# Kernel optimization log

Hardware: AMD Instinct MI355X
Metric: run time of the kernel (lower is better)

Reference implementation:

```python
import jax, jax.numpy as jnp
import numpy as np

HIDDEN = 3072
HEADS = 32
HEAD_DIM = HIDDEN // HEADS  # 96


def setup_inputs() -> dict:
    key = jax.random.key(0)
    k1, k2, k3, k4 = jax.random.split(key, 4)
    B, S = 2, 2048
    x = jax.random.normal(k1, (B, S, HIDDEN), dtype=jnp.float32)
    # qkv_proj: Linear(hidden, 3*hidden, bias=False); torch weight is [out,in]
    w_qkv = jax.random.normal(k2, (3 * HIDDEN, HIDDEN), dtype=jnp.float32) * (HIDDEN ** -0.5)
    # o_proj: Linear(hidden, hidden) with bias
    w_o = jax.random.normal(k3, (HIDDEN, HIDDEN), dtype=jnp.float32) * (HIDDEN ** -0.5)
    b_o = jax.random.normal(k4, (HIDDEN,), dtype=jnp.float32) * 0.01
    return {"x": x, "w_qkv": w_qkv, "w_o": w_o, "b_o": b_o}


def reference(x, w_qkv, w_o, b_o):
    B, S, _ = x.shape
    qkv = jnp.einsum('bsh,oh->bso', x, w_qkv)  # [B,S,3*HIDDEN]
    q, k, v = jnp.split(qkv, 3, axis=-1)
    # [B,S,HIDDEN] -> [B,H,S,D]
    def split_heads(t):
        return t.reshape(B, S, HEADS, HEAD_DIM).transpose(0, 2, 1, 3)
    q, k, v = split_heads(q), split_heads(k), split_heads(v)
    scores = jnp.einsum('bhqd,bhkd->bhqk', q, k) / jnp.sqrt(jnp.float32(HEAD_DIM))
    attn = jax.nn.softmax(scores, axis=-1)
    out = jnp.einsum('bhqk,bhkd->bhqd', attn, v)  # [B,H,S,D]
    out = out.transpose(0, 2, 1, 3).reshape(B, S, HIDDEN)
    return jnp.einsum('bsh,oh->bso', out, w_o) + b_o
```

## Files before the change

kernel.cpp:

```cpp
#include <hip/hip_runtime.h>
#include <math.h>


typedef unsigned int u32;
typedef unsigned short u16;
typedef __attribute__((ext_vector_type(8))) short bf16x8;
typedef __attribute__((ext_vector_type(4))) float f32x4;
typedef __attribute__((ext_vector_type(16))) float f32x16;

#define MFMA(a, b, c) __builtin_amdgcn_mfma_f32_16x16x32_bf16((a), (b), (c), 0, 0, 0)
#define MFMA32(a, b, c) __builtin_amdgcn_mfma_f32_32x32x16_bf16((a), (b), (c), 0, 0, 0)

#define GLDS16(g, l) __builtin_amdgcn_global_load_lds( \
    (const __attribute__((address_space(1))) u32*)(g), \
    (__attribute__((address_space(3))) u32*)(l), 16, 0, 0)

__device__ __forceinline__ u16 f2bf(float f) {
  u32 u = __builtin_bit_cast(u32, f);
  return (u16)((u + 0x7fffu + ((u >> 16) & 1u)) >> 16);
}
__device__ __forceinline__ float bf2f(u16 h) {
  u32 u = ((u32)h) << 16;
  return __builtin_bit_cast(float, u);
}
__device__ __forceinline__ void split2(float f, u16& h, u16& l) {
  h = f2bf(f);
  l = f2bf(f - bf2f(h));
}
__device__ __forceinline__ bf16x8 ld16(const u16* p) {
  return *reinterpret_cast<const bf16x8*>(p);
}

__global__ void split_kernel(const float* __restrict__ src, u16* __restrict__ dst,
                             long n) {
  long i = ((long)blockIdx.x * 256 + threadIdx.x) * 4;
  if (i >= n) return;
  const float4 v = *reinterpret_cast<const float4*>(src + i);
  const u32 i32 = (u32)i;
  const u32 row = i32 / 3072u;
  const u32 col = i32 - row * 3072u;
  const long base = (long)row * 6144 + (col >> 5) * 64 + (col & 31);
  ushort4 h, l;
  split2(v.x, h.x, l.x);
  split2(v.y, h.y, l.y);
  split2(v.z, h.z, l.z);
  split2(v.w, h.w, l.w);
  *reinterpret_cast<ushort4*>(dst + base) = h;
  *reinterpret_cast<ushort4*>(dst + base + 32) = l;
}

template <int MODE>
__global__ __launch_bounds__(256, 2) void gemm32(
    const u16* __restrict__ A2, const u16* __restrict__ B2,
    int M, int N, u16* __restrict__ C2, u16* __restrict__ Kp,
    u16* __restrict__ Vp, float* __restrict__ Cf, const float* __restrict__ bias) {
  constexpr int NT = 96;
  __shared__ u16 shm[2 * 128 * 64 + 2 * 192 * 64];
  u16* const uA = shm;
  u16* const uB = shm + 2 * 128 * 64;
  const int tid = threadIdx.x;
  const int lane = tid & 63;
  const int w = tid >> 6;
  const int wm = w >> 1, wn = w & 1;
  const int l31 = lane & 31;
  const int l5 = lane >> 5;

  const int mt = M >> 7;
  const int nwg = gridDim.x;
  const int bid = blockIdx.x;
  const int wg = (bid & 7) * (nwg >> 3) + (bid >> 3);
  const int bm = wg % mt, bn = wg / mt;

  const int srow = lane >> 3;
  const int sgc = ((lane & 7) ^ srow ^ w) * 8;

  auto stA = [&](int buf, int kt, int j) {
    const int r = j * 32 + w * 8 + srow;
    GLDS16(A2 + (long)(bm * 128 + r) * 6144 + kt * 64 + sgc,
           &uA[buf * 8192 + (j * 32 + w * 8) * 64]);
  };
  auto stB = [&](int buf, int kt, int j) {
    const int r = j * 32 + w * 8 + srow;
    GLDS16(B2 + (long)(bn * 192 + r) * 6144 + kt * 64 + sgc,
           &uB[buf * 12288 + (j * 32 + w * 8) * 64]);
  };

  f32x16 acc[2][3];
#pragma unroll
  for (int m = 0; m < 2; ++m)
#pragma unroll
    for (int n = 0; n < 3; ++n)
#pragma unroll
      for (int j = 0; j < 16; ++j) acc[m][n][j] = 0.f;

  stA(0, 0, 0); stA(0, 0, 1); stA(0, 0, 2); stA(0, 0, 3);
  stB(0, 0, 0); stB(0, 0, 1); stB(0, 0, 2);
  stB(0, 0, 3); stB(0, 0, 4); stB(0, 0, 5);
  __syncthreads();

  const int aRow0 = wm * 64 + l31;
  const int bRow0 = wn * 96 + l31;
  const int rk = (lane & 7) ^ ((lane >> 3) & 3);

#define CSLOT(KS, PL) ((((KS)*2 + l5 + (PL)*4) ^ rk) * 8)
#define RD_PH(KS)                                                          \
  _Pragma("unroll") for (int n = 0; n < 3; ++n) {                          \
    const int off = (bRow0 + n * 32) * 64;                                 \
    b[n][0] = ld16(&LB[off + CSLOT(KS, 0)]);                               \
    b[n][1] = ld16(&LB[off + CSLOT(KS, 1)]);                               \
  }                                                                        \
  _Pragma("unroll") for (int m = 0; m < 2; ++m) {                          \
    const int off = (aRow0 + m * 32) * 64;                                 \
    a[m][0] = ld16(&LA[off + CSLOT(KS, 0)]);                               \
    a[m][1] = ld16(&LA[off + CSLOT(KS, 1)]);                               \
  }
#define DO_MFMA3()                                                         \
  __builtin_amdgcn_s_setprio(1);                                           \
  _Pragma("unroll") for (int m = 0; m < 2; ++m)                            \
  _Pragma("unroll") for (int n = 0; n < 3; ++n) {                          \
    acc[m][n] = MFMA32(a[m][0], b[n][0], acc[m][n]);                       \
    acc[m][n] = MFMA32(a[m][0], b[n][1], acc[m][n]);                       \
    acc[m][n] = MFMA32(a[m][1], b[n][0], acc[m][n]);                       \
  }                                                                        \
  __builtin_amdgcn_s_setprio(0);
#define PH_SYNC()                                                          \
  __builtin_amdgcn_s_barrier();                                            \
  asm volatile("s_waitcnt lgkmcnt(0)" ::: "memory");                       \
  __builtin_amdgcn_sched_barrier(0);

  for (int t = 0; t < NT; ++t) {
    const int cur = t & 1;
    const int nxt = cur ^ 1;
    const u16* LA = &uA[cur * 8192];
    const u16* LB = &uB[cur * 12288];
    bf16x8 a[2][2], b[3][2];
    RD_PH(0);
    if (t + 1 < NT) {
      stA(nxt, t + 1, 0); stA(nxt, t + 1, 1);
      stA(nxt, t + 1, 2); stA(nxt, t + 1, 3);
      stB(nxt, t + 1, 0); stB(nxt, t + 1, 1); stB(nxt, t + 1, 2);
      stB(nxt, t + 1, 3); stB(nxt, t + 1, 4); stB(nxt, t + 1, 5);
    }
    PH_SYNC();
    DO_MFMA3();
    __builtin_amdgcn_s_barrier();
    RD_PH(1);
    PH_SYNC();
    DO_MFMA3();
    asm volatile("s_waitcnt vmcnt(0)" ::: "memory");
    __builtin_amdgcn_s_barrier();
  }
#undef CSLOT
#undef RD_PH
#undef DO_MFMA3
#undef PH_SYNC

  if (MODE == 1 || (MODE == 2 && bn < 16)) {
#pragma unroll
    for (int mf = 0; mf < 2; ++mf)
#pragma unroll
      for (int nf = 0; nf < 3; ++nf) {
        const int col = bn * 192 + wn * 96 + nf * 32 + l31;
#pragma unroll
        for (int reg = 0; reg < 16; ++reg) {
          const int rif = (reg & 3) + 8 * (reg >> 2) + 4 * l5;
          const long row = (long)bm * 128 + wm * 64 + mf * 32 + rif;
          const float v = acc[mf][nf][reg];
          if (MODE == 1) {
            Cf[row * N + col] = v + bias[col];
          } else {
            const long idx = row * 6144 + (col >> 5) * 64 + (col & 31);
            u16 h, l;
            split2(v, h, l);
            C2[idx] = h;
            C2[idx + 32] = l;
          }
        }
      }
  } else if (MODE == 2) {
    const bool isV = (bn >= 32);
    const int hd0 = (bn - (isV ? 32 : 16)) * 2;
    const int b = (bm * 128) >> 11;
    const int s_loc = (bm * 128) & 2047;
    u16* const P = shm;
    u16* const dst = isV ? Vp : Kp;
#pragma unroll
    for (int hf = 0; hf < 2; ++hf) {
      __syncthreads();
      if (wm == hf) {
#pragma unroll
        for (int mf = 0; mf < 2; ++mf)
#pragma unroll
          for (int nf = 0; nf < 3; ++nf)
#pragma unroll
            for (int reg = 0; reg < 16; ++reg) {
              const int rif = (reg & 3) + 8 * (reg >> 2) + 4 * l5;
              const int row_l = mf * 32 + rif;
              const int col_l = wn * 96 + nf * 32 + l31;
              u16 h, l;
              split2(acc[mf][nf][reg], h, l);
              P[row_l * 200 + col_l] = h;
              P[(64 + row_l) * 200 + col_l] = l;
            }
      }
      __syncthreads();
      const int lr = lane & 15, lg = lane >> 4;
      if (!isV) {
#pragma unroll
        for (int i = 0; i < 12; ++i) {
          const int ri = w * 12 + i;
          const int pl = ri & 1;
          const int kbi = (ri >> 1) & 3;
          const int c = (ri >> 3) % 3;
          const int hh = ri / 24;
          const bf16x8 v =
              ld16(&P[(pl * 64 + kbi * 16 + lr) * 200 + hh * 96 + c * 32 + lg * 8]);
          const int hl = b * 32 + hd0 + hh;
          const int kbg = ((s_loc + hf * 64) >> 4) + kbi;
          const long rec3 = ((long)hl * 128 + kbg) * 3 + c;
          *reinterpret_cast<bf16x8*>(dst + (rec3 * 2 + pl) * 512 + lane * 8) = v;
        }
      } else {
#pragma unroll
        for (int i = 0; i < 12; ++i) {
          const int ri = w * 12 + i;
          const int pl = ri & 1;
          const int kq = (ri >> 1) & 1;
          const int n = (ri >> 2) % 6;
          const int hh = ri / 24;
          bf16x8 v;
#pragma unroll
          for (int e = 0; e < 8; ++e)
            v[e] = (short)P[(pl * 64 + kq * 32 + lg * 8 + e) * 200 + hh * 96 + n * 16 + lr];
          const int hl = b * 32 + hd0 + hh;
          const int kqg = ((s_loc + hf * 64) >> 5) + kq;
          const long rec = (((long)hl * 6 + n) * 64 + kqg) * 2 + pl;
          *reinterpret_cast<bf16x8*>(dst + rec * 512 + lane * 8) = v;
        }
      }
    }
  }
}

__global__ __launch_bounds__(256, 2) void attn_kernel(
    const u16* __restrict__ Q2,
    const u16* __restrict__ Kp, const u16* __restrict__ Vp,
    u16* __restrict__ AO2) {
  __shared__ u16 kv[2][12 * 512];
  __shared__ u16 pb[4][2][2][512];
  const int lane = threadIdx.x & 63;
  const int wv = threadIdx.x >> 6;
  const int lr = lane & 15, lg = lane >> 4;

  const int nwg = gridDim.x;
  const int bid = blockIdx.x;
  const int wg = (bid & 7) * (nwg >> 3) + (bid >> 3);
  const int hl = wg >> 4;
  const int qblk = wg & 15;
  const int b = hl >> 5;
  const int q0 = qblk * 128 + wv * 32;

  bf16x8 qh[2][3], ql[2][3];
#pragma unroll
  for (int f = 0; f < 2; ++f) {
    const long qofs =
        ((long)(b * 2048 + q0 + f * 16 + lr)) * 6144 + ((hl & 31) * 3) * 64 + lg * 8;
#pragma unroll
    for (int c = 0; c < 3; ++c) {
      qh[f][c] = ld16(Q2 + qofs + c * 64);
      ql[f][c] = ld16(Q2 + qofs + c * 64 + 32);
    }
  }

  f32x4 o_acc[2][6];
#pragma unroll
  for (int f = 0; f < 2; ++f)
#pragma unroll
    for (int n = 0; n < 6; ++n)
#pragma unroll
      for (int j = 0; j < 4; ++j) o_acc[f][n][j] = 0.f;
  float lsum[2][4] = {{0.f, 0.f, 0.f, 0.f}, {0.f, 0.f, 0.f, 0.f}};

  const float scale = 0.10206207261596577f;

  auto stage = [&](int nb, int it) {
    const long kbase = ((long)hl * 768 + (long)it * 12) * 512;
#pragma unroll
    for (int j = 0; j < 3; ++j) {
      const int r = wv * 3 + j;
      const int tt = r / 6, rc = r % 6;
      GLDS16(Kp + kbase + ((long)(tt * 6 + rc)) * 512 + lane * 8,
             &kv[nb][r * 512]);
    }
  };

  stage(0, 0);
  __syncthreads();

  for (int it = 0; it < 64; ++it) {
    const int nb = it & 1;
    if (it < 63) stage(nb ^ 1, it + 1);
    const u16* L = kv[nb];

    bf16x8 vh[6], vl[6];
#pragma unroll
    for (int n = 0; n < 6; ++n) {
      const long ro = ((((long)(hl * 6 + n)) * 64 + it) * 2) * 512 + lane * 8;
      vh[n] = ld16(Vp + ro);
      vl[n] = ld16(Vp + ro + 512);
    }

    bf16x8 kh0[3], kl0[3], kh1[3], kl1[3];
#pragma unroll
    for (int c = 0; c < 3; ++c) {
      kh0[c] = ld16(L + (c * 2 + 0) * 512 + lane * 8);
      kl0[c] = ld16(L + (c * 2 + 1) * 512 + lane * 8);
      kh1[c] = ld16(L + (6 + c * 2 + 0) * 512 + lane * 8);
      kl1[c] = ld16(L + (6 + c * 2 + 1) * 512 + lane * 8);
    }

    bf16x8 pah[2], pal[2];
#pragma unroll
    for (int f = 0; f < 2; ++f) {
      f32x4 s0, s1;
#pragma unroll
      for (int j = 0; j < 4; ++j) { s0[j] = 0.f; s1[j] = 0.f; }
#pragma unroll
      for (int c = 0; c < 3; ++c) {
        s0 = MFMA(qh[f][c], kh0[c], s0);
        s1 = MFMA(qh[f][c], kh1[c], s1);
        s0 = MFMA(qh[f][c], kl0[c], s0);
        s1 = MFMA(qh[f][c], kl1[c], s1);
        s0 = MFMA(ql[f][c], kh0[c], s0);
        s1 = MFMA(ql[f][c], kh1[c], s1);
      }
      u16* pbh = pb[wv][f][0];
      u16* pbl = pb[wv][f][1];
#pragma unroll
      for (int j = 0; j < 4; ++j) {
        const float p0 = __expf(fmaf(s0[j], scale, -12.f));
        const float p1 = __expf(fmaf(s1[j], scale, -12.f));
        lsum[f][j] += p0 + p1;
        const int r = lg * 4 + j;
        const int key = j ^ lg;
        u16 h, l;
        split2(p0, h, l);
        const int a0 = r * 32 + ((((lr >> 3) ^ key) & 3) << 3) + (lr & 7);
        pbh[a0] = h;
        pbl[a0] = l;
        split2(p1, h, l);
        const int a1 = r * 32 + ((((2 + (lr >> 3)) ^ key) & 3) << 3) + (lr & 7);
        pbh[a1] = h;
        pbl[a1] = l;
      }
      const int rkey = (lr & 3) ^ (lr >> 2);
      const int ra = lr * 32 + (((lg ^ rkey) & 3) << 3);
      pah[f] = ld16(&pbh[ra]);
      pal[f] = ld16(&pbl[ra]);
    }

#pragma unroll
    for (int n = 0; n < 6; ++n)
#pragma unroll
      for (int f = 0; f < 2; ++f) {
        o_acc[f][n] = MFMA(pah[f], vh[n], o_acc[f][n]);
        o_acc[f][n] = MFMA(pah[f], vl[n], o_acc[f][n]);
        o_acc[f][n] = MFMA(pal[f], vh[n], o_acc[f][n]);
      }
    __syncthreads();
  }

#pragma unroll
  for (int f = 0; f < 2; ++f) {
    float inv[4];
#pragma unroll
    for (int j = 0; j < 4; ++j) {
      float rs = lsum[f][j];
#pragma unroll
      for (int mk = 1; mk < 16; mk <<= 1) rs += __shfl_xor(rs, mk);
      inv[j] = 1.f / rs;
    }
#pragma unroll
    for (int n = 0; n < 6; ++n)
#pragma unroll
      for (int j = 0; j < 4; ++j) {
        const long row = (long)(b * 2048 + q0 + f * 16 + lg * 4 + j);
        const long idx =
            row * 6144 + ((hl & 31) * 3 + (n >> 1)) * 64 + (n & 1) * 16 + lr;
        u16 h, l;
        split2(o_acc[f][n][j] * inv[j], h, l);
        AO2[idx] = h;
        AO2[idx + 32] = l;
      }
  }
}

extern "C" void kernel_launch(void* const* d_in, const int* in_sizes, int n_in,
                              void* d_out, int out_size, void* d_ws, size_t ws_size,
                              hipStream_t stream) {
  const float* x = (const float*)d_in[0];
  const float* wqkv = (const float*)d_in[1];
  const float* wo = (const float*)d_in[2];
  const float* bo = (const float*)d_in[3];
  float* out = (float*)d_out;
  char* ws = (char*)d_ws;

  const size_t E_X = (size_t)4096 * 3072;
  const size_t E_WQ = (size_t)9216 * 3072;
  const size_t E_WO = (size_t)3072 * 3072;

  u16* X2 = (u16*)ws;
  char* W0 = ws + 4 * E_X;
  u16* W2 = (u16*)W0;
  u16* Q2 = (u16*)(W0 + 4 * E_WQ);
  u16* KP = Q2 + 2 * E_X;
  u16* VP = KP + 2 * E_X;
  u16* AO2 = (u16*)W0;
  u16* WO2 = (u16*)(W0 + 4 * E_X);

  const size_t need = 4 * (4 * E_X + E_WQ);
  if (ws_size < need) return;

  split_kernel<<<12288, 256, 0, stream>>>(x, X2, (long)E_X);
  split_kernel<<<27648, 256, 0, stream>>>(wqkv, W2, (long)E_WQ);
  gemm32<2><<<1536, 256, 0, stream>>>(X2, W2, 4096, 9216, Q2, KP, VP,
                                      nullptr, nullptr);
  split_kernel<<<9216, 256, 0, stream>>>(wo, WO2, (long)E_WO);
  attn_kernel<<<1024, 256, 0, stream>>>(Q2, KP, VP, AO2);
  gemm32<1><<<512, 256, 0, stream>>>(AO2, WO2, 4096, 3072, nullptr, nullptr,
                                     nullptr, out, bo);
}
```

Before: 1.165 ms.

## Widen split kernel to 8 elements, split V loads, raise attention occupancy

The split kernel now handles 8 floats per thread and writes 16-byte hi/lo vectors, with half as many blocks launched. The attention kernel loads V in two halves of three column groups, each followed by its MFMAs, so fewer V registers are live at once. Its launch bounds move from 2 to 3 blocks per SIMD to raise occupancy. The tighter register cap risks spills, and the V loads now sit closer to their use, leaving less latency hiding.

```diff
diff --git a/kernel.cpp b/kernel.cpp
--- a/kernel.cpp
+++ b/kernel.cpp
@@ -33,20 +33,26 @@
 
 __global__ void split_kernel(const float* __restrict__ src, u16* __restrict__ dst,
                              long n) {
-  long i = ((long)blockIdx.x * 256 + threadIdx.x) * 4;
+  long i = ((long)blockIdx.x * 256 + threadIdx.x) * 8;
   if (i >= n) return;
-  const float4 v = *reinterpret_cast<const float4*>(src + i);
+  const float4 v0 = *reinterpret_cast<const float4*>(src + i);
+  const float4 v1 = *reinterpret_cast<const float4*>(src + i + 4);
   const u32 i32 = (u32)i;
   const u32 row = i32 / 3072u;
   const u32 col = i32 - row * 3072u;
   const long base = (long)row * 6144 + (col >> 5) * 64 + (col & 31);
-  ushort4 h, l;
-  split2(v.x, h.x, l.x);
-  split2(v.y, h.y, l.y);
-  split2(v.z, h.z, l.z);
-  split2(v.w, h.w, l.w);
-  *reinterpret_cast<ushort4*>(dst + base) = h;
-  *reinterpret_cast<ushort4*>(dst + base + 32) = l;
+  bf16x8 hv, lv;
+  u16 h, l;
+  split2(v0.x, h, l); hv[0] = (short)h; lv[0] = (short)l;
+  split2(v0.y, h, l); hv[1] = (short)h; lv[1] = (short)l;
+  split2(v0.z, h, l); hv[2] = (short)h; lv[2] = (short)l;
+  split2(v0.w, h, l); hv[3] = (short)h; lv[3] = (short)l;
+  split2(v1.x, h, l); hv[4] = (short)h; lv[4] = (short)l;
+  split2(v1.y, h, l); hv[5] = (short)h; lv[5] = (short)l;
+  split2(v1.z, h, l); hv[6] = (short)h; lv[6] = (short)l;
+  split2(v1.w, h, l); hv[7] = (short)h; lv[7] = (short)l;
+  *reinterpret_cast<bf16x8*>(dst + base) = hv;
+  *reinterpret_cast<bf16x8*>(dst + base + 32) = lv;
 }
 
 template <int MODE>
@@ -242,7 +248,7 @@
   }
 }
 
-__global__ __launch_bounds__(256, 2) void attn_kernel(
+__global__ __launch_bounds__(256, 3) void attn_kernel(
     const u16* __restrict__ Q2,
     const u16* __restrict__ Kp, const u16* __restrict__ Vp,
     u16* __restrict__ AO2) {
@@ -301,14 +307,6 @@
     const int nb = it & 1;
     if (it < 63) stage(nb ^ 1, it + 1);
     const u16* L = kv[nb];
-
-    bf16x8 vh[6], vl[6];
-#pragma unroll
-    for (int n = 0; n < 6; ++n) {
-      const long ro = ((((long)(hl * 6 + n)) * 64 + it) * 2) * 512 + lane * 8;
-      vh[n] = ld16(Vp + ro);
-      vl[n] = ld16(Vp + ro + 512);
-    }
 
     bf16x8 kh0[3], kl0[3], kh1[3], kl1[3];
 #pragma unroll
@@ -359,13 +357,34 @@
       pal[f] = ld16(&pbl[ra]);
     }
 
-#pragma unroll
-    for (int n = 0; n < 6; ++n)
+    bf16x8 vh[3], vl[3];
+#pragma unroll
+    for (int n = 0; n < 3; ++n) {
+      const long ro = ((((long)(hl * 6 + n)) * 64 + it) * 2) * 512 + lane * 8;
+      vh[n] = ld16(Vp + ro);
+      vl[n] = ld16(Vp + ro + 512);
+    }
+#pragma unroll
+    for (int n = 0; n < 3; ++n)
 #pragma unroll
       for (int f = 0; f < 2; ++f) {
         o_acc[f][n] = MFMA(pah[f], vh[n], o_acc[f][n]);
         o_acc[f][n] = MFMA(pah[f], vl[n], o_acc[f][n]);
         o_acc[f][n] = MFMA(pal[f], vh[n], o_acc[f][n]);
+      }
+#pragma unroll
+    for (int n = 0; n < 3; ++n) {
+      const long ro = ((((long)(hl * 6 + 3 + n)) * 64 + it) * 2) * 512 + lane * 8;
+      vh[n] = ld16(Vp + ro);
+      vl[n] = ld16(Vp + ro + 512);
+    }
+#pragma unroll
+    for (int n = 0; n < 3; ++n)
+#pragma unroll
+      for (int f = 0; f < 2; ++f) {
+        o_acc[f][3 + n] = MFMA(pah[f], vh[n], o_acc[f][3 + n]);
+        o_acc[f][3 + n] = MFMA(pah[f], vl[n], o_acc[f][3 + n]);
+        o_acc[f][3 + n] = MFMA(pal[f], vh[n], o_acc[f][3 + n]);
       }
     __syncthreads();
   }
@@ -421,11 +440,11 @@
   const size_t need = 4 * (4 * E_X + E_WQ);
   if (ws_size < need) return;
 
-  split_kernel<<<12288, 256, 0, stream>>>(x, X2, (long)E_X);
-  split_kernel<<<27648, 256, 0, stream>>>(wqkv, W2, (long)E_WQ);
+  split_kernel<<<6144, 256, 0, stream>>>(x, X2, (long)E_X);
+  split_kernel<<<13824, 256, 0, stream>>>(wqkv, W2, (long)E_WQ);
   gemm32<2><<<1536, 256, 0, stream>>>(X2, W2, 4096, 9216, Q2, KP, VP,
                                       nullptr, nullptr);
-  split_kernel<<<9216, 256, 0, stream>>>(wo, WO2, (long)E_WO);
+  split_kernel<<<4608, 256, 0, stream>>>(wo, WO2, (long)E_WO);
   attn_kernel<<<1024, 256, 0, stream>>>(Q2, KP, VP, AO2);
   gemm32<1><<<512, 256, 0, stream>>>(AO2, WO2, 4096, 3072, nullptr, nullptr,
                                      nullptr, out, bo);
```

New measurement: 1.335 ms. +14.6%, slower.
